# Kernel tuning notes

Hardware: AMD Instinct MI355X
Metric: run time of the kernel (lower is better)

Reference implementation:

```python
import jax, jax.numpy as jnp
import numpy as np

N = 100000
E = 3200000
IN_DIM = 128
HID = 128
OUT_DIM = 2
L = 3
P = 2
PART = IN_DIM // P  # 64, equals HID // P
G = 64  # number of graphs
EPS = 1e-5


def setup_inputs() -> dict:
    key = jax.random.key(0)
    ks = jax.random.split(key, 12)
    x = jax.random.normal(ks[0], (N, IN_DIM), dtype=jnp.float32)
    edge_index = jax.random.randint(ks[1], (2, E), 0, N, dtype=jnp.int64)
    batch = jnp.sort(jax.random.randint(ks[2], (N,), 0, G, dtype=jnp.int64))
    # stacked GCNConv params: all convs are PART->PART (64->64)
    W_conv = jax.random.normal(ks[3], (L, P, PART, PART), dtype=jnp.float32) * 0.1
    b_conv = jax.random.normal(ks[4], (L, P, PART), dtype=jnp.float32) * 0.02
    # batchnorm (eval mode, running stats)
    bn_gamma = jnp.ones((L, HID), dtype=jnp.float32) + 0.1 * jax.random.normal(ks[5], (L, HID))
    bn_beta = 0.1 * jax.random.normal(ks[6], (L, HID), dtype=jnp.float32)
    bn_mean = 0.1 * jax.random.normal(ks[7], (L, HID), dtype=jnp.float32)
    bn_var = jnp.ones((L, HID), dtype=jnp.float32) + 0.1 * jax.random.uniform(ks[8], (L, HID))
    W_fc1 = jax.random.normal(ks[9], (HID * L, HID), dtype=jnp.float32) * 0.05
    b_fc1 = jnp.zeros((HID,), dtype=jnp.float32)
    W_fc2 = jax.random.normal(ks[10], (HID, OUT_DIM), dtype=jnp.float32) * 0.05
    b_fc2 = jnp.zeros((OUT_DIM,), dtype=jnp.float32)
    return dict(x=x, edge_index=edge_index, batch=batch, W_conv=W_conv, b_conv=b_conv,
                bn_gamma=bn_gamma, bn_beta=bn_beta, bn_mean=bn_mean, bn_var=bn_var,
                W_fc1=W_fc1, b_fc1=b_fc1, W_fc2=W_fc2, b_fc2=b_fc2)


def _gcn_norm(edge_index, num_nodes):
    # add self loops, compute symmetric normalization (PyG gcn_norm, edge_weight=1)
    loop = jnp.arange(num_nodes, dtype=edge_index.dtype)
    row = jnp.concatenate([edge_index[0], loop])  # source j
    col = jnp.concatenate([edge_index[1], loop])  # target i
    deg = jax.ops.segment_sum(jnp.ones_like(col, dtype=jnp.float32), col, num_segments=num_nodes)
    dis = jnp.where(deg > 0, jax.lax.rsqrt(jnp.maximum(deg, 1.0)), 0.0)
    norm = dis[row] * dis[col]  # [E+N]
    return row, col, norm


def _gcn_conv(xp, W, b, row, col, norm, num_nodes):
    xw = xp @ W                               # [N, PART] linear first (PyG GCNConv)
    msg = xw[row] * norm[:, None]             # gather + scale
    out = jax.ops.segment_sum(msg, col, num_segments=num_nodes)  # scatter-add
    return out + b


def reference(x, edge_index, batch, W_conv, b_conv, bn_gamma, bn_beta, bn_mean, bn_var,
              W_fc1, b_fc1, W_fc2, b_fc2):
    num_nodes = x.shape[0]
    row, col, norm = _gcn_norm(edge_index, num_nodes)
    layer_outputs = []
    h = x
    for l in range(L):
        parts = jnp.split(h, P, axis=-1)
        outs = [_gcn_conv(parts[p], W_conv[l, p], b_conv[l, p], row, col, norm, num_nodes)
                for p in range(P)]
        h = jnp.concatenate(outs, axis=-1)  # [N, HID]
        # BatchNorm1d in eval mode
        h = (h - bn_mean[l]) * jax.lax.rsqrt(bn_var[l] + EPS) * bn_gamma[l] + bn_beta[l]
        h = jax.nn.relu(h)  # dropout inactive in eval
        layer_outputs.append(h)
    hjk = jnp.concatenate(layer_outputs, axis=-1)  # [N, HID*L]
    # global mean pool per graph
    sums = jax.ops.segment_sum(hjk, batch, num_segments=G)
    cnts = jax.ops.segment_sum(jnp.ones((num_nodes,), dtype=jnp.float32), batch, num_segments=G)
    pooled = sums / jnp.maximum(cnts, 1.0)[:, None]  # [G, HID*L]
    z = jax.nn.relu(pooled @ W_fc1 + b_fc1)
    z = z @ W_fc2 + b_fc2
    return jax.nn.log_softmax(z, axis=-1)
```

## Files before the change

kernel.cpp:

```cpp
#include <hip/hip_runtime.h>
#include <cstdint>
#include <cstddef>

#define FEAT 128
#define NLAYERS 3
#define EPS 1e-5f
#define TILE 8192
#define SBSHIFT 9

typedef unsigned int uint32;
typedef float floatx2 __attribute__((ext_vector_type(2)));

__global__ void scan1(const int* __restrict__ in, int* __restrict__ bsum, int n) {
  __shared__ int s[256];
  int t = threadIdx.x;
  int i = blockIdx.x * 256 + t;
  s[t] = (i < n) ? in[i] : 0;
  __syncthreads();
  for (int o = 128; o > 0; o >>= 1) {
    if (t < o) s[t] += s[t + o];
    __syncthreads();
  }
  if (t == 0) bsum[blockIdx.x] = s[0];
}

__global__ void scan2(int* __restrict__ bsum, int nb) {
  __shared__ int s[512];
  int t = threadIdx.x;
  int v = (t < nb) ? bsum[t] : 0;
  s[t] = v;
  __syncthreads();
  for (int o = 1; o < 512; o <<= 1) {
    int add = (t >= o) ? s[t - o] : 0;
    __syncthreads();
    s[t] += add;
    __syncthreads();
  }
  if (t < nb) bsum[t] = s[t] - v;
}

__global__ void gscan3(const int* __restrict__ in, const int* __restrict__ bsum,
                       int* __restrict__ out, int n) {
  __shared__ int s[256];
  int t = threadIdx.x;
  int i = blockIdx.x * 256 + t;
  int v = (i < n) ? in[i] : 0;
  s[t] = v;
  __syncthreads();
  for (int o = 1; o < 256; o <<= 1) {
    int add = (t >= o) ? s[t - o] : 0;
    __syncthreads();
    s[t] += add;
    __syncthreads();
  }
  if (i < n) out[i] = bsum[blockIdx.x] + s[t] - v;
}

__global__ __launch_bounds__(256) void l1count_k(const int* __restrict__ col,
                                                 int* __restrict__ C, int E, int NT,
                                                 int SB) {
  __shared__ int h[256];
  int t = threadIdx.x;
  h[t] = 0;
  __syncthreads();
  int base = blockIdx.x * TILE;
  int end = min(base + TILE, E);
  for (int i = base + t; i < end; i += 256) atomicAdd(&h[col[i] >> SBSHIFT], 1);
  __syncthreads();
  if (t < SB) C[t * NT + blockIdx.x] = h[t];
}

__global__ __launch_bounds__(256) void l1scatter_k(const int* __restrict__ row,
                                                   const int* __restrict__ col,
                                                   const int* __restrict__ Cex,
                                                   uint2* __restrict__ bbuf, int E, int NT,
                                                   int SB) {
  __shared__ int cur[256];
  int t = threadIdx.x;
  if (t < SB) cur[t] = Cex[t * NT + blockIdx.x];
  __syncthreads();
  int base = blockIdx.x * TILE;
  int end = min(base + TILE, E);
  for (int i = base + t; i < end; i += 256) {
    int c = col[i];
    int pos = atomicAdd(&cur[c >> SBSHIFT], 1);
    bbuf[pos] = make_uint2((uint32)row[i], (uint32)c);
  }
}

__global__ __launch_bounds__(256) void l2_k(const uint2* __restrict__ bbuf,
                                            const int* __restrict__ Cex,
                                            int* __restrict__ rowstart,
                                            float* __restrict__ dis,
                                            int* __restrict__ csrc,
                                            int N, int E, int NT, int SB) {
  __shared__ int hist[512];
  __shared__ int scanbuf[256];
  const int b = blockIdx.x;
  const int t = threadIdx.x;
  const int n0 = b << SBSHIFT;
  hist[t] = 0;
  hist[t + 256] = 0;
  __syncthreads();
  const int s = Cex[b * NT];
  const int e1 = (b == SB - 1) ? E : Cex[(b + 1) * NT];
  for (int i = s + t; i < e1; i += 256) {
    atomicAdd(&hist[bbuf[i].y & 511], 1);
  }
  __syncthreads();
  int a0 = hist[2 * t];
  int a1 = hist[2 * t + 1];
  int pair = a0 + a1;
  scanbuf[t] = pair;
  __syncthreads();
  for (int o = 1; o < 256; o <<= 1) {
    int add = (t >= o) ? scanbuf[t - o] : 0;
    __syncthreads();
    scanbuf[t] += add;
    __syncthreads();
  }
  int pairExcl = scanbuf[t] - pair;
  int c0 = s + pairExcl;
  int c1 = c0 + a0;
  int n = n0 + 2 * t;
  if (n < N) {
    rowstart[n] = c0;
    dis[n] = rsqrtf((float)(a0 + 1));
  }
  if (n + 1 < N) {
    rowstart[n + 1] = c1;
    dis[n + 1] = rsqrtf((float)(a1 + 1));
  }
  if (b == SB - 1 && t == 0) rowstart[N] = E;
  hist[2 * t] = c0;
  hist[2 * t + 1] = c1;
  __syncthreads();
  for (int i = s + t; i < e1; i += 256) {
    uint2 pk = bbuf[i];
    int pos = atomicAdd(&hist[pk.y & 511], 1);
    csrc[pos] = (int)pk.x;
  }
}

__global__ void boundaries_k(const int* __restrict__ batch, int* __restrict__ gstart,
                             int N, int G) {
  int n = blockIdx.x * blockDim.x + threadIdx.x;
  if (n >= N) return;
  int b = batch[n];
  int prev = (n == 0) ? -1 : batch[n - 1];
  for (int g = prev + 1; g <= b; ++g) gstart[g] = n;
  if (n == N - 1) {
    for (int g = b + 1; g <= G; ++g) gstart[g] = N;
  }
}

__global__ void bnprep_k(const float* __restrict__ bconv, const float* __restrict__ gamma,
                         const float* __restrict__ beta, const float* __restrict__ mean,
                         const float* __restrict__ var, float* __restrict__ bns,
                         float* __restrict__ bnt) {
  int l = blockIdx.x;
  int f = threadIdx.x;
  int i = l * FEAT + f;
  float s = gamma[i] * rsqrtf(var[i] + EPS);
  bns[i] = s;
  bnt[i] = (bconv[i] - mean[i]) * s + beta[i];
}

__global__ __launch_bounds__(256) void xw_k(const float* __restrict__ h,
                                            const float* __restrict__ W,
                                            const float* __restrict__ dis,
                                            uint32* __restrict__ xs8, int N) {
  __shared__ float hT[64 * 68];
  __shared__ float Ws[64 * 64];
  const int t = threadIdx.x;
  const int a = t >> 4;
  const int b = t & 15;
  const int base = blockIdx.x * 64;

  for (int p = 0; p < 2; ++p) {
    {
      const float4* src = (const float4*)(W + p * 4096);
      float4* dst = (float4*)Ws;
#pragma unroll
      for (int r = 0; r < 4; ++r) dst[r * 256 + t] = src[r * 256 + t];
    }
#pragma unroll
    for (int r = 0; r < 4; ++r) {
      int qid = r * 256 + t;
      int n = qid >> 4;
      int q = qid & 15;
      float4 v = make_float4(0.f, 0.f, 0.f, 0.f);
      int node = base + n;
      if (node < N) v = *(const float4*)(h + (size_t)node * FEAT + p * 64 + q * 4);
      hT[(q * 4 + 0) * 68 + n] = v.x;
      hT[(q * 4 + 1) * 68 + n] = v.y;
      hT[(q * 4 + 2) * 68 + n] = v.z;
      hT[(q * 4 + 3) * 68 + n] = v.w;
    }
    __syncthreads();

    float acc[4][4];
#pragma unroll
    for (int i = 0; i < 4; ++i)
#pragma unroll
      for (int j = 0; j < 4; ++j) acc[i][j] = 0.f;

#pragma unroll 8
    for (int k = 0; k < 64; ++k) {
      float4 hv = *(const float4*)(hT + k * 68 + a * 4);
      float4 wv = *(const float4*)(Ws + k * 64 + b * 4);
      acc[0][0] += hv.x * wv.x; acc[0][1] += hv.x * wv.y; acc[0][2] += hv.x * wv.z; acc[0][3] += hv.x * wv.w;
      acc[1][0] += hv.y * wv.x; acc[1][1] += hv.y * wv.y; acc[1][2] += hv.y * wv.z; acc[1][3] += hv.y * wv.w;
      acc[2][0] += hv.z * wv.x; acc[2][1] += hv.z * wv.y; acc[2][2] += hv.z * wv.z; acc[2][3] += hv.z * wv.w;
      acc[3][0] += hv.w * wv.x; acc[3][1] += hv.w * wv.y; acc[3][2] += hv.w * wv.z; acc[3][3] += hv.w * wv.w;
    }

#pragma unroll
    for (int i = 0; i < 4; ++i) {
      int node = base + a * 4 + i;
      if (node < N) {
        float d = dis[node];
        int w = __builtin_amdgcn_cvt_pk_fp8_f32(acc[i][0] * d, acc[i][1] * d, 0, false);
        w = __builtin_amdgcn_cvt_pk_fp8_f32(acc[i][2] * d, acc[i][3] * d, w, true);
        xs8[(size_t)node * 32 + p * 16 + b] = (uint32)w;
      }
    }
    __syncthreads();
  }
}

__global__ __launch_bounds__(256) void gather_k(const unsigned short* __restrict__ xs8,
                                                const float* __restrict__ dis,
                                                const int* __restrict__ rowstart,
                                                const int* __restrict__ csrc,
                                                const int* __restrict__ batch,
                                                const float* __restrict__ bns,
                                                const float* __restrict__ bnt,
                                                float* __restrict__ hout,
                                                float* __restrict__ sums,
                                                int layer, int N) {
  const int w = threadIdx.x >> 6;
  const int lane = threadIdx.x & 63;
  const int wid = blockIdx.x * 4 + w;
  const bool valid = (wid < N);
  const int f = lane * 2;

  float rx = 0.f, ry = 0.f;
  int g = -1;

  if (valid) {
    int e0 = rowstart[wid];
    int e1 = rowstart[wid + 1];
    float di = dis[wid];

    int selfv = xs8[(size_t)wid * 64 + lane];
    floatx2 sc = __builtin_amdgcn_cvt_pk_f32_fp8(selfv, false);
    float ax = sc[0];
    float ay = sc[1];

    for (int base = e0; base < e1; base += 64) {
      int cnt = min(64, e1 - base);
      int my = (lane < cnt) ? csrc[base + lane] : 0;
      int j = 0;
      for (; j + 7 < cnt; j += 8) {
        int s0 = __shfl(my, j);
        int s1 = __shfl(my, j + 1);
        int s2 = __shfl(my, j + 2);
        int s3 = __shfl(my, j + 3);
        int s4 = __shfl(my, j + 4);
        int s5 = __shfl(my, j + 5);
        int s6 = __shfl(my, j + 6);
        int s7 = __shfl(my, j + 7);
        int v0 = xs8[(size_t)s0 * 64 + lane];
        int v1 = xs8[(size_t)s1 * 64 + lane];
        int v2 = xs8[(size_t)s2 * 64 + lane];
        int v3 = xs8[(size_t)s3 * 64 + lane];
        int v4 = xs8[(size_t)s4 * 64 + lane];
        int v5 = xs8[(size_t)s5 * 64 + lane];
        int v6 = xs8[(size_t)s6 * 64 + lane];
        int v7 = xs8[(size_t)s7 * 64 + lane];
        floatx2 c0 = __builtin_amdgcn_cvt_pk_f32_fp8(v0, false);
        floatx2 c1 = __builtin_amdgcn_cvt_pk_f32_fp8(v1, false);
        floatx2 c2 = __builtin_amdgcn_cvt_pk_f32_fp8(v2, false);
        floatx2 c3 = __builtin_amdgcn_cvt_pk_f32_fp8(v3, false);
        floatx2 c4 = __builtin_amdgcn_cvt_pk_f32_fp8(v4, false);
        floatx2 c5 = __builtin_amdgcn_cvt_pk_f32_fp8(v5, false);
        floatx2 c6 = __builtin_amdgcn_cvt_pk_f32_fp8(v6, false);
        floatx2 c7 = __builtin_amdgcn_cvt_pk_f32_fp8(v7, false);
        ax += c0[0] + c1[0] + c2[0] + c3[0] + c4[0] + c5[0] + c6[0] + c7[0];
        ay += c0[1] + c1[1] + c2[1] + c3[1] + c4[1] + c5[1] + c6[1] + c7[1];
      }
      for (; j < cnt; ++j) {
        int s = __shfl(my, j);
        int v = xs8[(size_t)s * 64 + lane];
        floatx2 c = __builtin_amdgcn_cvt_pk_f32_fp8(v, false);
        ax += c[0];
        ay += c[1];
      }
    }
    ax *= di;
    ay *= di;
    rx = fmaxf(ax * bns[f] + bnt[f], 0.f);
    ry = fmaxf(ay * bns[f + 1] + bnt[f + 1], 0.f);
    if (hout) *(float2*)(hout + (size_t)wid * FEAT + f) = make_float2(rx, ry);
    g = batch[wid];
  }

  __shared__ float ps[4][FEAT];
  __shared__ int gs[4];
  if (lane == 0) gs[w] = g;
  *(float2*)&ps[w][f] = make_float2(rx, ry);
  __syncthreads();
  if (gs[0] >= 0 && gs[0] == gs[1] && gs[1] == gs[2] && gs[2] == gs[3]) {
    int t = threadIdx.x;
    if (t < FEAT) {
      float s = ps[0][t] + ps[1][t] + ps[2][t] + ps[3][t];
      atomicAdd(&sums[(size_t)gs[0] * (NLAYERS * FEAT) + layer * FEAT + t], s);
    }
  } else if (valid) {
    float* sp = sums + (size_t)g * (NLAYERS * FEAT) + layer * FEAT + f;
    atomicAdd(sp, rx);
    atomicAdd(sp + 1, ry);
  }
}

__global__ __launch_bounds__(128) void head_k(const float* __restrict__ sums,
                                              const int* __restrict__ gstart,
                                              const float* __restrict__ W1,
                                              const float* __restrict__ b1,
                                              const float* __restrict__ W2,
                                              const float* __restrict__ b2,
                                              float* __restrict__ out) {
  __shared__ float pooled[NLAYERS * FEAT];
  __shared__ float z1[FEAT];
  __shared__ float z2[2];
  int g = blockIdx.x;
  int t = threadIdx.x;
  float cnt = (float)(gstart[g + 1] - gstart[g]);
  float inv = 1.f / fmaxf(cnt, 1.f);
  for (int k = t; k < NLAYERS * FEAT; k += 128) pooled[k] = sums[g * (NLAYERS * FEAT) + k] * inv;
  __syncthreads();
  float acc = b1[t];
  for (int k = 0; k < NLAYERS * FEAT; ++k) acc += pooled[k] * W1[k * FEAT + t];
  z1[t] = fmaxf(acc, 0.f);
  __syncthreads();
  if (t < 2) {
    float a = b2[t];
    for (int j = 0; j < FEAT; ++j) a += z1[j] * W2[j * 2 + t];
    z2[t] = a;
  }
  __syncthreads();
  if (t < 2) {
    float m = fmaxf(z2[0], z2[1]);
    float lse = m + logf(expf(z2[0] - m) + expf(z2[1] - m));
    out[g * 2 + t] = z2[t] - lse;
  }
}


extern "C" void kernel_launch(void* const* d_in, const int* in_sizes, int n_in,
                              void* d_out, int out_size, void* d_ws, size_t ws_size,
                              hipStream_t stream) {
  const float* x    = (const float*)d_in[0];
  const int*   ei   = (const int*)d_in[1];
  const int*   batch= (const int*)d_in[2];
  const float* Wc   = (const float*)d_in[3];
  const float* bc   = (const float*)d_in[4];
  const float* gam  = (const float*)d_in[5];
  const float* bet  = (const float*)d_in[6];
  const float* mu   = (const float*)d_in[7];
  const float* var  = (const float*)d_in[8];
  const float* W1   = (const float*)d_in[9];
  const float* b1   = (const float*)d_in[10];
  const float* W2   = (const float*)d_in[11];
  const float* b2   = (const float*)d_in[12];
  float* out = (float*)d_out;

  const int N = in_sizes[0] / FEAT;
  const int E = in_sizes[1] / 2;
  const int G = out_size / 2;
  const int SB = (N + (1 << SBSHIFT) - 1) >> SBSHIFT;
  const int NT = (E + TILE - 1) / TILE;

  const int* row = ei;
  const int* col = ei + E;

  char* p = (char*)d_ws;
  auto alloc = [&](size_t bytes) -> void* {
    void* q = (void*)p;
    p += (bytes + 255) & ~(size_t)255;
    return q;
  };
  float*  dis      = (float*)alloc((size_t)N * 4);
  int*    rowstart = (int*)alloc((size_t)(N + 1) * 4);
  int*    csrc     = (int*)alloc((size_t)E * 4);
  int*    bsum     = (int*)alloc(1024 * 4);
  int*    gstart   = (int*)alloc(1024 * 4);
  int*    C        = (int*)alloc((size_t)256 * NT * 4);
  float*  bns      = (float*)alloc(NLAYERS * FEAT * 4);
  float*  bnt      = (float*)alloc(NLAYERS * FEAT * 4);
  float*  sums     = (float*)alloc((size_t)G * NLAYERS * FEAT * 4);
  uint32* bufA     = (uint32*)alloc((size_t)N * FEAT);
  float*  bufB     = (float*)alloc((size_t)N * FEAT * 4);
  uint2*  bbuf     = (uint2*)bufB;

  const int nbN = (N + 255) / 256;
  const int Csz = SB * NT;
  const int nbC = (Csz + 255) / 256;

  hipMemsetAsync(sums, 0, (size_t)G * NLAYERS * FEAT * 4, stream);

  l1count_k<<<NT, 256, 0, stream>>>(col, C, E, NT, SB);
  scan1<<<nbC, 256, 0, stream>>>(C, bsum, Csz);
  scan2<<<1, 512, 0, stream>>>(bsum, nbC);
  gscan3<<<nbC, 256, 0, stream>>>(C, bsum, C, Csz);
  l1scatter_k<<<NT, 256, 0, stream>>>(row, col, C, bbuf, E, NT, SB);
  l2_k<<<SB, 256, 0, stream>>>(bbuf, C, rowstart, dis, csrc, N, E, NT, SB);

  boundaries_k<<<nbN, 256, 0, stream>>>(batch, gstart, N, G);
  bnprep_k<<<NLAYERS, FEAT, 0, stream>>>(bc, gam, bet, mu, var, bns, bnt);

  const int xwBlocks = (N + 63) / 64;
  const int gaBlocks = (N + 3) / 4;
  const float* hin = x;
  for (int l = 0; l < NLAYERS; ++l) {
    xw_k<<<xwBlocks, 256, 0, stream>>>(hin, Wc + (size_t)l * 8192, dis, bufA, N);
    float* hptr = (l == NLAYERS - 1) ? nullptr : bufB;
    gather_k<<<gaBlocks, 256, 0, stream>>>((const unsigned short*)bufA, dis, rowstart,
                                           csrc, batch, bns + l * FEAT, bnt + l * FEAT,
                                           hptr, sums, l, N);
    hin = bufB;
  }

  head_k<<<G, 128, 0, stream>>>(sums, gstart, W1, b1, W2, b2, out);
}
```

Baseline: 644.1 us.

## Store intermediate activations as bf16 and pack CSR bucket entries into 32 bits

Layer outputs between GCN layers are now written as packed bf16 pairs and unpacked in the xw kernel. This halves the activation write and read traffic. The edge bucketing buffer now packs the source row (17 bits) and local column (9 bits) into one 32-bit word instead of a uint2, halving scatter and bucketing bandwidth. The bf16 storage lowers activation precision, and the packing assumes node indices fit in 17 bits.

Result: no change. 638.3 us (-0.9%).

```diff
diff --git a/kernel.cpp b/kernel.cpp
--- a/kernel.cpp
+++ b/kernel.cpp
@@ -11,6 +11,14 @@
 typedef unsigned int uint32;
 typedef float floatx2 __attribute__((ext_vector_type(2)));
 
+__device__ __forceinline__ uint32 pack_bf16(float a, float b) {
+  uint32 ua = __float_as_uint(a);
+  uint32 ub = __float_as_uint(b);
+  ua += 0x7fffu + ((ua >> 16) & 1u);
+  ub += 0x7fffu + ((ub >> 16) & 1u);
+  return (ua >> 16) | (ub & 0xffff0000u);
+}
+
 __global__ void scan1(const int* __restrict__ in, int* __restrict__ bsum, int n) {
   __shared__ int s[256];
   int t = threadIdx.x;
@@ -73,7 +81,7 @@
 __global__ __launch_bounds__(256) void l1scatter_k(const int* __restrict__ row,
                                                    const int* __restrict__ col,
                                                    const int* __restrict__ Cex,
-                                                   uint2* __restrict__ bbuf, int E, int NT,
+                                                   uint32* __restrict__ bbuf, int E, int NT,
                                                    int SB) {
   __shared__ int cur[256];
   int t = threadIdx.x;
@@ -84,11 +92,11 @@
   for (int i = base + t; i < end; i += 256) {
     int c = col[i];
     int pos = atomicAdd(&cur[c >> SBSHIFT], 1);
-    bbuf[pos] = make_uint2((uint32)row[i], (uint32)c);
-  }
-}
-
-__global__ __launch_bounds__(256) void l2_k(const uint2* __restrict__ bbuf,
+    bbuf[pos] = ((uint32)(c & ((1 << SBSHIFT) - 1)) << 17) | (uint32)row[i];
+  }
+}
+
+__global__ __launch_bounds__(256) void l2_k(const uint32* __restrict__ bbuf,
                                             const int* __restrict__ Cex,
                                             int* __restrict__ rowstart,
                                             float* __restrict__ dis,
@@ -105,7 +113,7 @@
   const int s = Cex[b * NT];
   const int e1 = (b == SB - 1) ? E : Cex[(b + 1) * NT];
   for (int i = s + t; i < e1; i += 256) {
-    atomicAdd(&hist[bbuf[i].y & 511], 1);
+    atomicAdd(&hist[bbuf[i] >> 17], 1);
   }
   __syncthreads();
   int a0 = hist[2 * t];
@@ -136,9 +144,9 @@
   hist[2 * t + 1] = c1;
   __syncthreads();
   for (int i = s + t; i < e1; i += 256) {
-    uint2 pk = bbuf[i];
-    int pos = atomicAdd(&hist[pk.y & 511], 1);
-    csrc[pos] = (int)pk.x;
+    uint32 pk = bbuf[i];
+    int pos = atomicAdd(&hist[pk >> 17], 1);
+    csrc[pos] = (int)(pk & 0x1FFFFu);
   }
 }
 
@@ -166,7 +174,7 @@
   bnt[i] = (bconv[i] - mean[i]) * s + beta[i];
 }
 
-__global__ __launch_bounds__(256) void xw_k(const float* __restrict__ h,
+__global__ __launch_bounds__(256) void xw_k(const void* __restrict__ h, int isBf16,
                                             const float* __restrict__ W,
                                             const float* __restrict__ dis,
                                             uint32* __restrict__ xs8, int N) {
@@ -191,7 +199,17 @@
       int q = qid & 15;
       float4 v = make_float4(0.f, 0.f, 0.f, 0.f);
       int node = base + n;
-      if (node < N) v = *(const float4*)(h + (size_t)node * FEAT + p * 64 + q * 4);
+      if (node < N) {
+        if (isBf16) {
+          uint2 wv = *(const uint2*)((const uint32*)h + (size_t)node * 64 + p * 32 + q * 2);
+          v.x = __uint_as_float(wv.x << 16);
+          v.y = __uint_as_float(wv.x & 0xffff0000u);
+          v.z = __uint_as_float(wv.y << 16);
+          v.w = __uint_as_float(wv.y & 0xffff0000u);
+        } else {
+          v = *(const float4*)((const float*)h + (size_t)node * FEAT + p * 64 + q * 4);
+        }
+      }
       hT[(q * 4 + 0) * 68 + n] = v.x;
       hT[(q * 4 + 1) * 68 + n] = v.y;
       hT[(q * 4 + 2) * 68 + n] = v.z;
@@ -236,7 +254,7 @@
                                                 const int* __restrict__ batch,
                                                 const float* __restrict__ bns,
                                                 const float* __restrict__ bnt,
-                                                float* __restrict__ hout,
+                                                uint32* __restrict__ hout,
                                                 float* __restrict__ sums,
                                                 int layer, int N) {
   const int w = threadIdx.x >> 6;
@@ -302,7 +320,7 @@
     ay *= di;
     rx = fmaxf(ax * bns[f] + bnt[f], 0.f);
     ry = fmaxf(ay * bns[f + 1] + bnt[f + 1], 0.f);
-    if (hout) *(float2*)(hout + (size_t)wid * FEAT + f) = make_float2(rx, ry);
+    if (hout) hout[(size_t)wid * 64 + lane] = pack_bf16(rx, ry);
     g = batch[wid];
   }
 
@@ -401,8 +419,8 @@
   float*  bnt      = (float*)alloc(NLAYERS * FEAT * 4);
   float*  sums     = (float*)alloc((size_t)G * NLAYERS * FEAT * 4);
   uint32* bufA     = (uint32*)alloc((size_t)N * FEAT);
-  float*  bufB     = (float*)alloc((size_t)N * FEAT * 4);
-  uint2*  bbuf     = (uint2*)bufB;
+  uint32* bufB     = (uint32*)alloc((size_t)N * 64 * 4);
+  uint32* bbuf     = (uint32*)bufB;
 
   const int nbN = (N + 255) / 256;
   const int Csz = SB * NT;
@@ -422,14 +440,16 @@
 
   const int xwBlocks = (N + 63) / 64;
   const int gaBlocks = (N + 3) / 4;
-  const float* hin = x;
+  const void* hin = (const void*)x;
+  int isBf16 = 0;
   for (int l = 0; l < NLAYERS; ++l) {
-    xw_k<<<xwBlocks, 256, 0, stream>>>(hin, Wc + (size_t)l * 8192, dis, bufA, N);
-    float* hptr = (l == NLAYERS - 1) ? nullptr : bufB;
+    xw_k<<<xwBlocks, 256, 0, stream>>>(hin, isBf16, Wc + (size_t)l * 8192, dis, bufA, N);
+    uint32* hptr = (l == NLAYERS - 1) ? nullptr : bufB;
     gather_k<<<gaBlocks, 256, 0, stream>>>((const unsigned short*)bufA, dis, rowstart,
                                            csrc, batch, bns + l * FEAT, bnt + l * FEAT,
                                            hptr, sums, l, N);
-    hin = bufB;
+    hin = (const void*)bufB;
+    isBf16 = 1;
   }
 
   head_k<<<G, 128, 0, stream>>>(sums, gstart, W1, b1, W2, b2, out);
```
